# Kernel optimization log

Measured on AMD Instinct MI355X. Metric: run time of the kernel, lower is better.

Reference implementation:

```python
import jax, jax.numpy as jnp
import numpy as np

C = 256
H = W = 80
PATCH = 3  # patchsize, stride 1 -> npatches = (H-2)*(W-2) = 6084


def setup_inputs() -> dict:
    key = jax.random.key(0)
    k_style, k_x = jax.random.split(key)
    style = jax.random.normal(k_style, (1, C, H, W), jnp.float32)
    # torch: activation.unfold(2,3,1).unfold(3,3,1).squeeze() -> (C, nH, nW, 3, 3)
    #        .permute(1,2,0,3,4).view(nH*nW, C, 3, 3)
    s = np.asarray(style)
    win = np.lib.stride_tricks.sliding_window_view(s, (PATCH, PATCH), axis=(2, 3))  # (1,C,78,78,3,3)
    patches = np.ascontiguousarray(win[0].transpose(1, 2, 0, 3, 4).reshape(-1, C, PATCH, PATCH))
    x = jax.random.normal(k_x, (1, C, H, W), jnp.float32)
    return {"x": x, "patches": jnp.asarray(patches)}


def reference(x, patches):
    # NOTE: the original's per-patch normalization uses .mul (not .mul_), a no-op,
    # so conv_enc weight == raw patches, same as conv_dec. Replicated here.
    npatches = patches.shape[0]
    dn = ("NCHW", "OIHW", "NCHW")
    # conv_enc: valid 3x3 conv, patches as filters -> (1, npatches, 78, 78)
    sim = jax.lax.conv_general_dilated(x, patches, (1, 1), "VALID", dimension_numbers=dn)
    # per-pixel argmax over patch channel + one-hot (replaces the python double loop)
    idx = jnp.argmax(sim, axis=1)  # (1, 78, 78)
    onehot = jax.nn.one_hot(idx, npatches, axis=1, dtype=x.dtype)  # (1, npatches, 78, 78)
    # conv_dec / aux: ConvTranspose2d == adjoint of the valid conv (transpose_kernel=True)
    swap = jax.lax.conv_transpose(onehot, patches, (1, 1), "VALID", dimension_numbers=dn, transpose_kernel=True)
    swap_wei = jax.lax.conv_transpose(onehot, jnp.ones_like(patches), (1, 1), "VALID", dimension_numbers=dn, transpose_kernel=True)
    return swap / swap_wei  # (1, C, 80, 80)
```

## Files before the change

kernel.cpp:

```cpp
#include <hip/hip_runtime.h>
#include <stdint.h>

#define NPIX 6084
#define NPAD 6144
#define KDIM 2304
#define KB   (KDIM*2)

typedef __attribute__((ext_vector_type(8))) short s16x8;
typedef __attribute__((ext_vector_type(4))) float f32x4;

__device__ __forceinline__ short f2bf(float f) {
  unsigned u = __builtin_bit_cast(unsigned, f);
  u += 0x7FFFu + ((u >> 16) & 1u);
  return (short)(u >> 16);
}
__device__ __forceinline__ float bf2f(short s) {
  unsigned u = ((unsigned)(unsigned short)s) << 16;
  return __builtin_bit_cast(float, u);
}

#define GL16(g, l)                                                            \
  __builtin_amdgcn_global_load_lds(                                           \
      (__attribute__((address_space(1))) unsigned int*)(g),                   \
      (__attribute__((address_space(3))) unsigned int*)(l), 16, 0, 0)

__global__ __launch_bounds__(256) void k_prep_pat(const float* __restrict__ pat,
                                                  short* __restrict__ out) {
  int i = blockIdx.x * 256 + threadIdx.x;
  int e0 = i * 8;
  int row = e0 / KDIM;
  s16x8 v;
  if (row < NPIX) {
    const float* s = pat + e0;
#pragma unroll
    for (int j = 0; j < 8; ++j) v[j] = f2bf(s[j]);
  } else {
#pragma unroll
    for (int j = 0; j < 8; ++j) v[j] = 0;
  }
  *(s16x8*)(out + e0) = v;
}

__global__ __launch_bounds__(256) void k_prep_xcol(const float* __restrict__ x,
                                                   short* __restrict__ out) {
  int i = blockIdx.x * 256 + threadIdx.x;
  int e0 = i * 8;
  int m = e0 / KDIM;
  int k0 = e0 - m * KDIM;
  s16x8 v;
  if (m < NPIX) {
    int p = m / 78, q = m - p * 78;
#pragma unroll
    for (int j = 0; j < 8; ++j) {
      int k = k0 + j;
      int c = k / 9;
      int r = k - c * 9;
      int dy = r / 3, dx = r - dy * 3;
      v[j] = f2bf(x[c * 6400 + (p + dy) * 80 + (q + dx)]);
    }
  } else {
#pragma unroll
    for (int j = 0; j < 8; ++j) v[j] = 0;
  }
  *(s16x8*)(out + e0) = v;
}

__global__ __launch_bounds__(256) void k_gemm(const short* __restrict__ A,
                                              const short* __restrict__ B,
                                              short* __restrict__ C) {
  __shared__ short As[128 * 32];
  __shared__ short Bs[128 * 32];
  const int tid = threadIdx.x;
  const int w = tid >> 6, lane = tid & 63;
  const int wr = w >> 1, wc = w & 1;
  const int tm = blockIdx.y, tn = blockIdx.x;
  const char* Ab = (const char*)A + (size_t)tm * 128 * KB;
  const char* Bb = (const char*)B + (size_t)tn * 128 * KB;
  const int r0 = lane >> 2;
  const int kbyte = (lane & 3) * 16;
  f32x4 acc[4][4] = {};

  const short* ap = &As[(wr * 64 + (lane & 15)) * 32 + (lane >> 4) * 8];
  const short* bp = &Bs[(wc * 64 + (lane & 15)) * 32 + (lane >> 4) * 8];

  for (int kk = 0; kk < KDIM; kk += 32) {
#pragma unroll
    for (int o = 0; o < 2; ++o) {
      int ch = o * 4 + w;
      int r = ch * 16 + r0;
      GL16(Ab + (size_t)r * KB + kk * 2 + kbyte, &As[ch * 512]);
      GL16(Bb + (size_t)r * KB + kk * 2 + kbyte, &Bs[ch * 512]);
    }
    asm volatile("s_waitcnt vmcnt(0)" ::: "memory");
    __syncthreads();
    s16x8 a[4], b[4];
#pragma unroll
    for (int i = 0; i < 4; ++i) a[i] = *(const s16x8*)(ap + i * 512);
#pragma unroll
    for (int i = 0; i < 4; ++i) b[i] = *(const s16x8*)(bp + i * 512);
#pragma unroll
    for (int mi = 0; mi < 4; ++mi)
#pragma unroll
      for (int ni = 0; ni < 4; ++ni)
        acc[mi][ni] = __builtin_amdgcn_mfma_f32_16x16x32_bf16(
            a[mi], b[ni], acc[mi][ni], 0, 0, 0);
    __syncthreads();
  }

  const int rowb = tm * 128 + wr * 64 + (lane >> 4) * 4;
  const int colb = tn * 128 + wc * 64 + (lane & 15);
#pragma unroll
  for (int mi = 0; mi < 4; ++mi)
#pragma unroll
    for (int ni = 0; ni < 4; ++ni)
#pragma unroll
      for (int j = 0; j < 4; ++j)
        C[(size_t)(rowb + mi * 16 + j) * NPAD + colb + ni * 16] =
            f2bf(acc[mi][ni][j]);
}

__global__ __launch_bounds__(256) void k_argmax(const short* __restrict__ sim,
                                                const float* __restrict__ x,
                                                const float* __restrict__ pat,
                                                int* __restrict__ amax) {
  __shared__ int cand[4][32];
  __shared__ int ccnt[4];
  const int tid = threadIdx.x, w = tid >> 6, lane = tid & 63;
  const int pix = blockIdx.x * 4 + w;
  const short* row = sim + (size_t)pix * NPAD;

  float best = -1e30f;
  int bidx = 0;
  for (int it = 0; it < 12; ++it) {
    int k0 = (it * 64 + lane) * 8;
    if (k0 < NPIX) {
      s16x8 v = *(const s16x8*)(row + k0);
#pragma unroll
      for (int j = 0; j < 8; ++j) {
        int k = k0 + j;
        float f = bf2f(v[j]);
        if (k < NPIX && (f > best || (f == best && k < bidx))) {
          best = f; bidx = k;
        }
      }
    }
  }
  for (int off = 32; off; off >>= 1) {
    float ov = __shfl_down(best, off);
    int oi = __shfl_down(bidx, off);
    if (ov > best || (ov == best && oi < bidx)) { best = ov; bidx = oi; }
  }
  float maxv = __shfl(best, 0);

  if (lane == 0) ccnt[w] = 0;
  __syncthreads();

  const float thr = maxv - 4.0f;
  for (int it = 0; it < 12; ++it) {
    int k0 = (it * 64 + lane) * 8;
    if (k0 < NPIX) {
      s16x8 v = *(const s16x8*)(row + k0);
#pragma unroll
      for (int j = 0; j < 8; ++j) {
        int k = k0 + j;
        float f = bf2f(v[j]);
        if (k < NPIX && f >= thr) {
          int pos = atomicAdd(&ccnt[w], 1);
          if (pos < 32) cand[w][pos] = k;
        }
      }
    }
  }
  __syncthreads();

  int n = ccnt[w] < 32 ? ccnt[w] : 32;
  const int p = pix / 78, q = pix - (pix / 78) * 78;
  double bests = -1e300;
  int bestk = 0;
  for (int ci = 0; ci < n; ++ci) {
    int k = cand[w][ci];
    double s = 0.0;
    for (int cc = lane; cc < 256; cc += 64) {
      const float* xb = x + cc * 6400 + p * 80 + q;
      const float* pb = pat + (size_t)k * KDIM + cc * 9;
#pragma unroll
      for (int dy = 0; dy < 3; ++dy)
#pragma unroll
        for (int dx = 0; dx < 3; ++dx)
          s += (double)xb[dy * 80 + dx] * (double)pb[dy * 3 + dx];
    }
    for (int off = 32; off; off >>= 1) s += __shfl_down(s, off);
    if (lane == 0 && (s > bests || (s == bests && k < bestk))) {
      bests = s; bestk = k;
    }
  }
  if (lane == 0) amax[pix] = bestk;
}

__global__ __launch_bounds__(256) void k_scat9(const float* __restrict__ pat,
                                               const int* __restrict__ amax,
                                               float* __restrict__ plane) {
  __shared__ float lp[KDIM];
  const int b = blockIdx.x;
  const int k = amax[b];
  const int p = b / 78, q = b - (b / 78) * 78;
  const float* src = pat + (size_t)k * KDIM;
#pragma unroll
  for (int j = 0; j < 9; ++j) lp[j * 256 + threadIdx.x] = src[j * 256 + threadIdx.x];
  __syncthreads();
  const int c = threadIdx.x;
#pragma unroll
  for (int r = 0; r < 9; ++r) {
    int dy = r / 3, dx = r - dy * 3;
    int pos = (p + dy) * 80 + (q + dx);
    plane[(size_t)r * 1638400 + pos * 256 + c] = lp[c * 9 + r];
  }
}

__global__ __launch_bounds__(256) void k_reduce(const float* __restrict__ plane,
                                                float* __restrict__ out) {
  const int c = threadIdx.x;
  const int pix0 = blockIdx.x * 16;
  for (int i = 0; i < 16; ++i) {
    int pix = pix0 + i;
    int yy = pix / 80, xx = pix - (pix / 80) * 80;
    float s = 0.f;
    int cnt = 0;
#pragma unroll
    for (int r = 0; r < 9; ++r) {
      int dy = r / 3, dx = r - dy * 3;
      int p = yy - dy, q = xx - dx;
      if (p >= 0 && p < 78 && q >= 0 && q < 78) {
        s += plane[(size_t)r * 1638400 + pix * 256 + c];
        ++cnt;
      }
    }
    out[c * 6400 + pix] = s / (float)cnt;
  }
}

extern "C" void kernel_launch(void* const* d_in, const int* in_sizes, int n_in,
                              void* d_out, int out_size, void* d_ws,
                              size_t ws_size, hipStream_t stream) {
  const float* x = (const float*)d_in[0];
  const float* pat = (const float*)d_in[1];
  float* out = (float*)d_out;
  char* ws = (char*)d_ws;

  short* patB = (short*)ws;
  short* xcol = (short*)(ws + 28311552);
  short* sim  = (short*)(ws + 2 * 28311552);
  float* plane = (float*)sim;
  int*   amax = (int*)(ws + 2 * 28311552 + 75497472);

  k_prep_pat<<<6912, 256, 0, stream>>>(pat, patB);
  k_prep_xcol<<<6912, 256, 0, stream>>>(x, xcol);
  k_gemm<<<dim3(48, 48), 256, 0, stream>>>(xcol, patB, sim);
  k_argmax<<<1521, 256, 0, stream>>>(sim, x, pat, amax);
  k_scat9<<<6084, 256, 0, stream>>>(pat, amax, plane);
  k_reduce<<<400, 256, 0, stream>>>(plane, out);
}
```

Baseline: 459.4 us.

## Rewrite GEMM as 256x256 tile, 8-wave, double-buffered swizzled-LDS pipeline

Replaces the 128x128, 4-wave bf16 GEMM with a 256x256 tile on 512 threads using 128 KB of LDS split into two stages, with XOR-swizzled layouts. Global-to-LDS loads for the next K-tiles are interleaved with MFMA quadrants and partial vmcnt waits, and setprio is raised around MFMA bursts. This aims to raise arithmetic intensity and hide load latency that the old single-buffered loop exposed. The cost is heavy LDS use, which limits occupancy, more complex synchronisation, and a 576-block grid that can leave CUs unevenly loaded.

```diff
diff --git a/kernel.cpp b/kernel.cpp
--- a/kernel.cpp
+++ b/kernel.cpp
@@ -5,6 +5,7 @@
 #define NPAD 6144
 #define KDIM 2304
 #define KB   (KDIM*2)
+#define NT   36
 
 typedef __attribute__((ext_vector_type(8))) short s16x8;
 typedef __attribute__((ext_vector_type(4))) float f32x4;
@@ -65,52 +66,108 @@
   *(s16x8*)(out + e0) = v;
 }
 
-__global__ __launch_bounds__(256) void k_gemm(const short* __restrict__ A,
-                                              const short* __restrict__ B,
-                                              short* __restrict__ C) {
-  __shared__ short As[128 * 32];
-  __shared__ short Bs[128 * 32];
+__global__ __launch_bounds__(512, 2) void k_gemm(const short* __restrict__ A,
+                                                 const short* __restrict__ B,
+                                                 short* __restrict__ C) {
+  __shared__ __align__(1024) char smem[131072];
   const int tid = threadIdx.x;
   const int w = tid >> 6, lane = tid & 63;
-  const int wr = w >> 1, wc = w & 1;
+  const int wr = w >> 2, wc = w & 3;
   const int tm = blockIdx.y, tn = blockIdx.x;
-  const char* Ab = (const char*)A + (size_t)tm * 128 * KB;
-  const char* Bb = (const char*)B + (size_t)tn * 128 * KB;
-  const int r0 = lane >> 2;
-  const int kbyte = (lane & 3) * 16;
-  f32x4 acc[4][4] = {};
-
-  const short* ap = &As[(wr * 64 + (lane & 15)) * 32 + (lane >> 4) * 8];
-  const short* bp = &Bs[(wc * 64 + (lane & 15)) * 32 + (lane >> 4) * 8];
-
-  for (int kk = 0; kk < KDIM; kk += 32) {
-#pragma unroll
-    for (int o = 0; o < 2; ++o) {
-      int ch = o * 4 + w;
-      int r = ch * 16 + r0;
-      GL16(Ab + (size_t)r * KB + kk * 2 + kbyte, &As[ch * 512]);
-      GL16(Bb + (size_t)r * KB + kk * 2 + kbyte, &Bs[ch * 512]);
-    }
-    asm volatile("s_waitcnt vmcnt(0)" ::: "memory");
-    __syncthreads();
-    s16x8 a[4], b[4];
-#pragma unroll
-    for (int i = 0; i < 4; ++i) a[i] = *(const s16x8*)(ap + i * 512);
-#pragma unroll
-    for (int i = 0; i < 4; ++i) b[i] = *(const s16x8*)(bp + i * 512);
-#pragma unroll
-    for (int mi = 0; mi < 4; ++mi)
-#pragma unroll
-      for (int ni = 0; ni < 4; ++ni)
-        acc[mi][ni] = __builtin_amdgcn_mfma_f32_16x16x32_bf16(
-            a[mi], b[ni], acc[mi][ni], 0, 0, 0);
-    __syncthreads();
-  }
-
-  const int rowb = tm * 128 + wr * 64 + (lane >> 4) * 4;
-  const int colb = tn * 128 + wc * 64 + (lane & 15);
-#pragma unroll
-  for (int mi = 0; mi < 4; ++mi)
+  const char* Ab = (const char*)A + (size_t)tm * 256 * KB;
+  const char* Bb = (const char*)B + (size_t)tn * 256 * KB;
+
+  const int srccol = ((lane & 7) * 16) ^ (lane & 32);
+  const int lrow = lane >> 3;
+  const int fragRow = lane & 15;
+  const int fragCol = ((lane >> 4) * 16) ^ (((lane >> 2) & 1) << 5);
+  const int aOff = (wr * 128 + fragRow) * 128 + fragCol;
+  const int bOff = 32768 + (wc * 64 + fragRow) * 128 + fragCol;
+
+  f32x4 acc[8][4] = {};
+  s16x8 a[4][2];
+  s16x8 b[2][2][2];
+
+#define STAGE_A(par, hs, kt)                                                  \
+  _Pragma("unroll") for (int j = 0; j < 2; ++j) {                             \
+    int c = w * 2 + j;                                                        \
+    int rb = (c < 8) ? (hs)*64 + c * 8 : 128 + (hs)*64 + (c - 8) * 8;         \
+    GL16(Ab + (size_t)(rb + lrow) * KB + (kt)*128 + srccol,                   \
+         smem + (par)*65536 + rb * 128);                                      \
+  }
+#define STAGE_B(par, hs, kt)                                                  \
+  _Pragma("unroll") for (int j = 0; j < 2; ++j) {                             \
+    int c = w * 2 + j;                                                        \
+    int rb = (c >> 2) * 64 + (hs)*32 + (c & 3) * 8;                           \
+    GL16(Bb + (size_t)(rb + lrow) * KB + (kt)*128 + srccol,                   \
+         smem + (par)*65536 + 32768 + rb * 128);                              \
+  }
+#define LDA(par, mh)                                                          \
+  _Pragma("unroll") for (int mi2 = 0; mi2 < 4; ++mi2)                         \
+  _Pragma("unroll") for (int ks = 0; ks < 2; ++ks)                            \
+    a[mi2][ks] = *(const s16x8*)(smem + (par)*65536 + aOff + (mh)*8192 +      \
+                                 mi2 * 2048 + ks * 64);
+#define LDB(par, nh)                                                          \
+  _Pragma("unroll") for (int ni2 = 0; ni2 < 2; ++ni2)                         \
+  _Pragma("unroll") for (int ks = 0; ks < 2; ++ks)                            \
+    b[nh][ni2][ks] = *(const s16x8*)(smem + (par)*65536 + bOff + (nh)*4096 +  \
+                                     ni2 * 2048 + ks * 64);
+#define VM6() asm volatile("s_waitcnt vmcnt(6)" ::: "memory")
+#define BAR() asm volatile("s_barrier" ::: "memory")
+#define BARL() asm volatile("s_barrier\n\ts_waitcnt lgkmcnt(0)" ::: "memory")
+#define QM(mh, nh)                                                            \
+  do {                                                                        \
+    __builtin_amdgcn_s_setprio(1);                                            \
+    _Pragma("unroll") for (int mi2 = 0; mi2 < 4; ++mi2)                       \
+    _Pragma("unroll") for (int ni2 = 0; ni2 < 2; ++ni2)                       \
+    _Pragma("unroll") for (int ks = 0; ks < 2; ++ks)                          \
+      acc[(mh)*4 + mi2][(nh)*2 + ni2] =                                       \
+          __builtin_amdgcn_mfma_f32_16x16x32_bf16(                            \
+              a[mi2][ks], b[nh][ni2][ks], acc[(mh)*4 + mi2][(nh)*2 + ni2],    \
+              0, 0, 0);                                                       \
+    __builtin_amdgcn_s_setprio(0);                                            \
+    BAR();                                                                    \
+  } while (0)
+
+  STAGE_A(0, 0, 0); STAGE_B(0, 0, 0); STAGE_B(0, 1, 0); STAGE_A(0, 1, 0);
+  STAGE_A(1, 0, 1); STAGE_B(1, 0, 1); STAGE_B(1, 1, 1);
+  VM6();
+  BAR();
+
+#pragma unroll 1
+  for (int i = 0; i < NT / 2; ++i) {
+    const int t2 = (2 * i + 2 < NT) ? 2 * i + 2 : NT - 1;
+    const int t3 = (2 * i + 3 < NT) ? 2 * i + 3 : NT - 1;
+    LDA(0, 0); LDB(0, 0);
+    STAGE_A(1, 1, 2 * i + 1);
+    BARL(); QM(0, 0);
+    LDB(0, 1);
+    STAGE_A(0, 0, t2);
+    BARL(); QM(0, 1);
+    LDA(0, 1);
+    STAGE_B(0, 0, t2);
+    BARL(); QM(1, 1);
+    STAGE_B(0, 1, t2);
+    VM6();
+    BARL(); QM(1, 0);
+    LDA(1, 0); LDB(1, 0);
+    STAGE_A(0, 1, t2);
+    BARL(); QM(0, 0);
+    LDB(1, 1);
+    STAGE_A(1, 0, t3);
+    BARL(); QM(0, 1);
+    LDA(1, 1);
+    STAGE_B(1, 0, t3);
+    BARL(); QM(1, 1);
+    STAGE_B(1, 1, t3);
+    VM6();
+    BARL(); QM(1, 0);
+  }
+
+  const int rowb = tm * 256 + wr * 128 + (lane >> 4) * 4;
+  const int colb = tn * 256 + wc * 64 + (lane & 15);
+#pragma unroll
+  for (int mi = 0; mi < 8; ++mi)
 #pragma unroll
     for (int ni = 0; ni < 4; ++ni)
 #pragma unroll
@@ -255,7 +312,7 @@
 
   k_prep_pat<<<6912, 256, 0, stream>>>(pat, patB);
   k_prep_xcol<<<6912, 256, 0, stream>>>(x, xcol);
-  k_gemm<<<dim3(48, 48), 256, 0, stream>>>(xcol, patB, sim);
+  k_gemm<<<dim3(24, 24), 512, 0, stream>>>(xcol, patB, sim);
   k_argmax<<<1521, 256, 0, stream>>>(sim, x, pat, amax);
   k_scat9<<<6084, 256, 0, stream>>>(pat, amax, plane);
   k_reduce<<<400, 256, 0, stream>>>(plane, out);
```

Result: no change. 456.5 us (-0.6%).
